# Optimization experiments

Hardware: AMD Instinct MI355X
Metric: run time of the kernel (lower is better)

## Reference

```python
import jax, jax.numpy as jnp
from jax import lax
import numpy as np

B, OBS, PRED, F, H = 2048, 20, 30, 16, 1024


def _lstm_layer(x, Wih, Whh, bih, bhh):
    # x: [T, B, in]; PyTorch gate order i, f, g, o; zero initial state
    Bb = x.shape[1]
    Hh = Whh.shape[1]
    def step(carry, xt):
        h, c = carry
        g = xt @ Wih.T + h @ Whh.T + bih + bhh
        i, f, gg, o = jnp.split(g, 4, axis=-1)
        c = jax.nn.sigmoid(f) * c + jax.nn.sigmoid(i) * jnp.tanh(gg)
        h = jax.nn.sigmoid(o) * jnp.tanh(c)
        return (h, c), h
    z = jnp.zeros((Bb, Hh), x.dtype)
    _, hs = lax.scan(step, (z, z), x)
    return hs  # [T, B, H]


def _lstm2(x, Wih0, Whh0, bih0, bhh0, Wih1, Whh1, bih1, bhh1):
    return _lstm_layer(_lstm_layer(x, Wih0, Whh0, bih0, bhh0), Wih1, Whh1, bih1, bhh1)


def setup_inputs() -> dict:
    key = jax.random.key(0)
    ks = jax.random.split(key, 32)
    s = 0.05
    def w(k, shape):
        return jax.random.normal(k, shape, dtype=jnp.float32) * s
    d = {
        'x_in': jax.random.normal(ks[0], (B, OBS, F), dtype=jnp.float32),
        'y': jax.random.normal(ks[1], (B, PRED, F), dtype=jnp.float32),
        'v_in': jax.random.normal(ks[2], (B, OBS, F), dtype=jnp.float32),
        'sx': jnp.ones((1,), jnp.float32),
        'sv': jnp.ones((1,), jnp.float32),
    }
    i = 3
    for p in ['v', 'a']:
        d[p + 'Wih0'] = w(ks[i], (4 * H, F)); i += 1
        d[p + 'Whh0'] = w(ks[i], (4 * H, H)); i += 1
        d[p + 'bih0'] = w(ks[i], (4 * H,)); i += 1
        d[p + 'bhh0'] = w(ks[i], (4 * H,)); i += 1
        d[p + 'Wih1'] = w(ks[i], (4 * H, H)); i += 1
        d[p + 'Whh1'] = w(ks[i], (4 * H, H)); i += 1
        d[p + 'bih1'] = w(ks[i], (4 * H,)); i += 1
        d[p + 'bhh1'] = w(ks[i], (4 * H,)); i += 1
        d[p + 'Wl'] = w(ks[i], (F, H)); i += 1
        d[p + 'bl'] = w(ks[i], (F,)); i += 1
    return d


def reference(x_in, y, v_in, sx, sv,
              vWih0, vWhh0, vbih0, vbhh0, vWih1, vWhh1, vbih1, vbhh1, vWl, vbl,
              aWih0, aWhh0, abih0, abhh0, aWih1, aWhh1, abih1, abhh1, aWl, abl):
    # last observed position, scaled: [1, B, F]
    x = jnp.transpose(x_in, (1, 0, 2))[-1:] * sx
    yT = sx * jnp.transpose(y, (1, 0, 2))  # [PRED, B, F]
    v_seq = jnp.transpose(v_in, (1, 0, 2))  # [OBS, B, F]
    a_seq = v_seq[1:] - v_seq[:-1]          # [OBS-1, B, F]

    vh = _lstm2(v_seq, vWih0, vWhh0, vbih0, vbhh0, vWih1, vWhh1, vbih1, vbhh1)
    v = sv * jnp.tanh(vh[-1:] @ vWl.T + vbl)  # [1, B, F]

    ah = _lstm2(a_seq, aWih0, aWhh0, abih0, abhh0, aWih1, aWhh1, abih1, abhh1)
    a = jnp.tanh(ah @ aWl.T + abl)[-1:]       # [1, B, F] (unscaled, fed back)

    v = v + sv * a
    x = x + v

    def body(carry, _):
        a, v, x = carry
        # NOTE: faithful to source -- LSTM state resets to zero each step
        ah = _lstm2(a, aWih0, aWhh0, abih0, abhh0, aWih1, aWhh1, abih1, abhh1)
        a = jnp.tanh(ah @ aWl.T + abl)
        v = v + sv * a
        x = x + v
        return (a, v, x), x[0]

    _, xs = lax.scan(body, (a, v, x), None, length=PRED - 1)  # xs: [PRED-1, B, F]
    out = jnp.concatenate([x, xs], axis=0)  # [PRED, B, F]
    return (out, yT)
```

## Files before the change

kernel.cpp:

```cpp
#include <hip/hip_runtime.h>


#define B_    2048
#define OBS_  20
#define PRED_ 30
#define F_    16
#define H_    1024
#define GN_   4096

typedef _Float16 f16;
typedef _Float16 f16x8 __attribute__((ext_vector_type(8)));
typedef _Float16 f16x4 __attribute__((ext_vector_type(4)));
typedef float    f32x4 __attribute__((ext_vector_type(4)));

__device__ __forceinline__ float fast_sigmoid(float x) {
  return 1.0f / (1.0f + __expf(-x));
}
__device__ __forceinline__ float fast_tanh(float x) {
  float ax = fabsf(x);
  float e  = __expf(-2.0f * ax);
  float r  = (1.0f - e) / (1.0f + e);
  return copysignf(r, x);
}

__device__ __forceinline__ void stageA512(f16* dst, const f16* Asrc, int b0, int k0, int tid) {
  int o  = tid * 16;
  int rr = o >> 6;
  int sp = (o >> 4) & 3;
  int sl = sp ^ ((rr >> 1) & 3);
  const f16* gp = Asrc + (size_t)(b0 + rr) * H_ + k0 + sl * 8;
  __builtin_amdgcn_global_load_lds(
      (const __attribute__((address_space(1))) void*)gp,
      (__attribute__((address_space(3))) void*)((char*)dst + o), 16, 0, 0);
}
__device__ __forceinline__ void stageB512(f16* dst, const f16* Wsrc, int j0, int k0, int tid) {
#pragma unroll
  for (int cc = 0; cc < 2; ++cc) {
    int o  = cc * 8192 + tid * 16;
    int rr = o >> 6;
    int sp = (o >> 4) & 3;
    int sl = sp ^ ((rr >> 1) & 3);
    int grow = (rr >> 6) * H_ + j0 + (rr & 63);
    const f16* gp = Wsrc + (size_t)grow * H_ + k0 + sl * 8;
    __builtin_amdgcn_global_load_lds(
        (const __attribute__((address_space(1))) void*)gp,
        (__attribute__((address_space(3))) void*)((char*)dst + o), 16, 0, 0);
  }
}

__device__ __forceinline__ void acc_init(f32x4 (&acc)[4][4], const float* bias, int jcol) {
#pragma unroll
  for (int g = 0; g < 4; ++g) {
    float bv = bias[g * H_ + jcol];
#pragma unroll
    for (int m = 0; m < 4; ++m) acc[m][g] = (f32x4){bv, bv, bv, bv};
  }
}

__device__ __forceinline__ void run_k16(f32x4 (&acc)[4][4], const f16* A16, const f16* W16,
    int b0, int j0, int wr, int wc, int lcol, int lkq)
{
  f16x8 za = {0, 0, 0, 0, 0, 0, 0, 0};
  f16x8 af[4], bf[4];
#pragma unroll
  for (int m = 0; m < 4; ++m) {
    if (lkq < 2) {
      int row = b0 + wr * 64 + m * 16 + lcol;
      af[m] = *(const f16x8*)(A16 + (size_t)row * 16 + lkq * 8);
    } else af[m] = za;
  }
#pragma unroll
  for (int g = 0; g < 4; ++g) {
    if (lkq < 2) {
      int row = g * H_ + j0 + wc * 16 + lcol;
      bf[g] = *(const f16x8*)(W16 + (size_t)row * 16 + lkq * 8);
    } else bf[g] = za;
  }
#pragma unroll
  for (int m = 0; m < 4; ++m)
#pragma unroll
    for (int g = 0; g < 4; ++g)
      acc[m][g] = __builtin_amdgcn_mfma_f32_16x16x32_f16(af[m], bf[g], acc[m][g], 0, 0, 0);
}

__device__ __forceinline__ void kstep_mfma(f32x4 (&acc)[4][4], const f16* lA, const f16* lB,
    int wr, int wc, int lcol, int lkq)
{
  f16x8 av[4], bw[4];
#pragma unroll
  for (int m = 0; m < 4; ++m) {
    int ar = wr * 64 + m * 16 + lcol;
    int sa = lkq ^ ((ar >> 1) & 3);
    av[m] = *(const f16x8*)&lA[ar * 32 + sa * 8];
  }
#pragma unroll
  for (int g = 0; g < 4; ++g) {
    int br = g * 64 + wc * 16 + lcol;
    int sb = lkq ^ ((br >> 1) & 3);
    bw[g] = *(const f16x8*)&lB[br * 32 + sb * 8];
  }
#pragma unroll
  for (int m = 0; m < 4; ++m)
#pragma unroll
    for (int g = 0; g < 4; ++g)
      acc[m][g] = __builtin_amdgcn_mfma_f32_16x16x32_f16(av[m], bw[g], acc[m][g], 0, 0, 0);
}

__device__ __forceinline__ void run_kloop(f32x4 (&acc)[4][4],
    f16 (*lA)[4096], f16 (*lB)[8192],
    const f16* A0, const f16* W0, const f16* A1, const f16* W1,
    int NT, int NTSW,
    int b0, int j0, int tid, int wr, int wc, int lcol, int lkq)
{
  int cur = 0;
  for (int t = 0; t < NT; ++t) {
    if (t + 1 < NT) {
      int tn = t + 1;
      const f16* As = (tn >= NTSW) ? A1 : A0;
      const f16* Ws = (tn >= NTSW) ? W1 : W0;
      int k0 = (tn & 31) * 32;
      stageA512(lA[cur ^ 1], As, b0, k0, tid);
      stageB512(lB[cur ^ 1], Ws, j0, k0, tid);
      asm volatile("s_waitcnt vmcnt(3)\n\ts_barrier" ::: "memory");
    } else {
      asm volatile("s_waitcnt vmcnt(0)\n\ts_barrier" ::: "memory");
    }
    kstep_mfma(acc, lA[cur], lB[cur], wr, wc, lcol, lkq);
    asm volatile("s_waitcnt lgkmcnt(0)\n\ts_barrier" ::: "memory");
    cur ^= 1;
  }
}

__device__ __forceinline__ void lstm_epi_g(f32x4 (&acc)[4][4], const float* cin, float* cout,
    f16* hout, int b0, int jcol, int wr, int lkq, int hasc, int writec)
{
#pragma unroll
  for (int m = 0; m < 4; ++m) {
    int brow0 = b0 + wr * 64 + m * 16 + lkq * 4;
#pragma unroll
    for (int r = 0; r < 4; ++r) {
      size_t bi = (size_t)(brow0 + r) * H_ + jcol;
      float gi = acc[m][0][r], gf = acc[m][1][r], gg = acc[m][2][r], go = acc[m][3][r];
      float cold = hasc ? cin[bi] : 0.0f;
      float cn = fast_sigmoid(gf) * cold + fast_sigmoid(gi) * fast_tanh(gg);
      float hv = fast_sigmoid(go) * fast_tanh(cn);
      if (writec) cout[bi] = cn;
      hout[bi] = (f16)hv;
    }
  }
}

struct StepArgs {
  const f16* A16; const f16* W16v; const f16* W16a;
  const f16* A0;  const f16* W0v;  const f16* W0a;
  const f16* A1;  const f16* W1v;  const f16* W1a;
  const float* bv; const float* ba;
  const float* cin; float* cout; f16* hout;
  int k16, nt, hasc, writec;
};

__device__ __forceinline__ void lstm_body(const StepArgs& p, f16 (*lA)[4096], f16 (*lB)[8192], int bi)
{
  const int tid = threadIdx.x, lane = tid & 63;
  const int wv = tid >> 6;
  const int wr = wv >> 2, wc = wv & 3;
  const int bm = bi >> 4, bn = bi & 15;
  const int b0 = bm * 128, j0 = bn * 64;
  const int ch = bm >> 4;
  const int lcol = lane & 15, lkq = lane >> 4;
  const int jcol = j0 + wc * 16 + lcol;

  const f16* W16 = ch ? p.W16a : p.W16v;
  const f16* W0  = ch ? p.W0a  : p.W0v;
  const f16* W1  = ch ? p.W1a  : p.W1v;
  const float* bias = ch ? p.ba : p.bv;

  if (p.nt) { stageA512(lA[0], p.A0, b0, 0, tid); stageB512(lB[0], W0, j0, 0, tid); }
  f32x4 acc[4][4];
  acc_init(acc, bias, jcol);
  if (p.k16) run_k16(acc, p.A16, W16, b0, j0, wr, wc, lcol, lkq);
  if (p.nt)
    run_kloop(acc, lA, lB, p.A0, W0, p.A1, W1, p.nt, 32, b0, j0, tid, wr, wc, lcol, lkq);
  lstm_epi_g(acc, p.cin, p.cout, p.hout, b0, jcol, wr, lkq, p.hasc, p.writec);
}

__global__ __launch_bounds__(512, 4)
void obs_pair(StepArgs rlong, StepArgs qshort, int split)
{
  __shared__ f16 lA[2][4096];
  __shared__ f16 lB[2][8192];
  int blk = blockIdx.x;
  if (blk < split) lstm_body(rlong, lA, lB, blk);
  else             lstm_body(qshort, lA, lB, blk - split);
}

__global__ __launch_bounds__(512, 2)
void scan_l1(const f16* __restrict__ h0, const f16* __restrict__ Wih1,
             const float* __restrict__ bias1, const float* __restrict__ Wl,
             float* __restrict__ ppart)
{
  __shared__ f16 lA[2][4096];
  __shared__ f16 lB[2][8192];
  __shared__ f16 hl[128 * 72];
  const int tid = threadIdx.x, lane = tid & 63;
  const int wv = tid >> 6;
  const int wr = wv >> 2, wc = wv & 3;
  const int bm = blockIdx.x >> 4, bn = blockIdx.x & 15;
  const int b0 = bm * 128, j0 = bn * 64;
  const int lcol = lane & 15, lkq = lane >> 4;
  const int jcol = j0 + wc * 16 + lcol;

  stageA512(lA[0], h0, b0, 0, tid);
  stageB512(lB[0], Wih1, j0, 0, tid);
  f32x4 acc[4][4];
  acc_init(acc, bias1, jcol);
  run_kloop(acc, lA, lB, h0, Wih1, nullptr, nullptr, 32, 32, b0, j0, tid, wr, wc, lcol, lkq);

  int jl = wc * 16 + lcol;
#pragma unroll
  for (int m = 0; m < 4; ++m) {
#pragma unroll
    for (int r = 0; r < 4; ++r) {
      int row = wr * 64 + m * 16 + lkq * 4 + r;
      float gi = acc[m][0][r], gg = acc[m][2][r], go = acc[m][3][r];
      float cn = fast_sigmoid(gi) * fast_tanh(gg);
      float hv = fast_sigmoid(go) * fast_tanh(cn);
      hl[row * 72 + jl] = (f16)hv;
    }
  }
  __syncthreads();

  const float* wp = Wl + (size_t)lcol * H_ + j0 + lkq * 8;
  f16x8 bf0, bf1;
#pragma unroll
  for (int e = 0; e < 8; ++e) { bf0[e] = (f16)wp[e]; bf1[e] = (f16)wp[32 + e]; }
  int arow = wv * 16 + lcol;
  f16x8 af0 = *(const f16x8*)&hl[arow * 72 + lkq * 8];
  f16x8 af1 = *(const f16x8*)&hl[arow * 72 + 32 + lkq * 8];
  f32x4 pc = {0, 0, 0, 0};
  pc = __builtin_amdgcn_mfma_f32_16x16x32_f16(af0, bf0, pc, 0, 0, 0);
  pc = __builtin_amdgcn_mfma_f32_16x16x32_f16(af1, bf1, pc, 0, 0, 0);
#pragma unroll
  for (int r = 0; r < 4; ++r) {
    int prow = b0 + wv * 16 + lkq * 4 + r;
    ppart[(size_t)prow * 256 + bn * 16 + lcol] = pc[r];
  }
}

template<int FIRST, int LAST>
__global__ __launch_bounds__(256, 4)
void scan_l0(const float* __restrict__ ppart, const f16* __restrict__ a16f,
             const float* __restrict__ bl, const float* __restrict__ sv,
             float* __restrict__ v_buf, float* __restrict__ x_buf,
             float* __restrict__ out_t,
             const float* __restrict__ bias0, const f16* __restrict__ Wih0,
             f16* __restrict__ h0out)
{
  __shared__ f16 a_lds[128 * 16];
  const int tid = threadIdx.x;
  const int bm = LAST ? (int)blockIdx.x : (int)(blockIdx.x >> 5);
  const int bn = LAST ? 0 : (int)(blockIdx.x & 31);
  const int b0 = bm * 128;

  const int ebase = tid * 8;
  const int erow  = ebase >> 4;
  const int ef0   = ebase & 15;
  float av[8];
  if (FIRST) {
    f16x8 a8 = *(const f16x8*)&a16f[(size_t)(b0 + erow) * 16 + ef0];
#pragma unroll
    for (int e = 0; e < 8; ++e) av[e] = (float)a8[e];
  } else {
    f32x4 s0 = {0, 0, 0, 0}, s1 = {0, 0, 0, 0};
    const float* pp = ppart + (size_t)(b0 + erow) * 256 + ef0;
#pragma unroll
    for (int sN = 0; sN < 16; ++sN) {
      s0 += *(const f32x4*)(pp + sN * 16);
      s1 += *(const f32x4*)(pp + sN * 16 + 4);
    }
#pragma unroll
    for (int e = 0; e < 4; ++e) av[e] = fast_tanh(s0[e] + bl[ef0 + e]);
#pragma unroll
    for (int e = 0; e < 4; ++e) av[4 + e] = fast_tanh(s1[e] + bl[ef0 + 4 + e]);
    if (bn == 0) {
      float svv = sv[0];
#pragma unroll
      for (int e = 0; e < 8; ++e) {
        int idx = (b0 + erow) * F_ + ef0 + e;
        float v = v_buf[idx] + svv * av[e];
        v_buf[idx] = v;
        float x = x_buf[idx] + v;
        x_buf[idx] = x;
        out_t[idx] = x;
      }
    }
  }

  if (!LAST) {
    f16x8 a8;
#pragma unroll
    for (int e = 0; e < 8; ++e) a8[e] = (f16)av[e];
    *(f16x8*)&a_lds[ebase] = a8;
    __syncthreads();

    const int lane = tid & 63;
    const int wv = tid >> 6, wr = wv >> 1, wc = wv & 1;
    const int lcol = lane & 15, lkq = lane >> 4;
    const int j0 = bn * 32, jcol = j0 + wc * 16 + lcol;
    f32x4 acc[4][4];
    acc_init(acc, bias0, jcol);
    f16x8 za = {0, 0, 0, 0, 0, 0, 0, 0};
    f16x8 af[4], bf[4];
#pragma unroll
    for (int m = 0; m < 4; ++m) {
      if (lkq < 2) {
        int arow = wr * 64 + m * 16 + lcol;
        af[m] = *(const f16x8*)&a_lds[arow * 16 + lkq * 8];
      } else af[m] = za;
    }
#pragma unroll
    for (int g = 0; g < 4; ++g) {
      if (lkq < 2) {
        int brow = g * H_ + j0 + wc * 16 + lcol;
        bf[g] = *(const f16x8*)(Wih0 + (size_t)brow * 16 + lkq * 8);
      } else bf[g] = za;
    }
#pragma unroll
    for (int m = 0; m < 4; ++m)
#pragma unroll
      for (int g = 0; g < 4; ++g)
        acc[m][g] = __builtin_amdgcn_mfma_f32_16x16x32_f16(af[m], bf[g], acc[m][g], 0, 0, 0);
    lstm_epi_g(acc, nullptr, nullptr, h0out, b0, jcol, wr, lkq, 0, 0);
  }
}

template<int MODE>
__global__ __launch_bounds__(256)
void proj_update(const f16* __restrict__ h1, const float* __restrict__ Wl,
                 const float* __restrict__ bl, const float* __restrict__ sv,
                 float* __restrict__ v_buf, float* __restrict__ x_buf,
                 float* __restrict__ out_t, f16* __restrict__ a16)
{
  __shared__ f16 lh[16 * 1024];
  const int b0r = blockIdx.x * 16;
  const int tid = threadIdx.x;
#pragma unroll
  for (int c = 0; c < 8; ++c) {
    int o = c * 256 + tid;
    *(f16x8*)&lh[o * 8] = *(const f16x8*)&h1[(size_t)b0r * 1024 + o * 8];
  }
  __syncthreads();
  const int br = tid >> 4;
  const int f  = tid & 15;
  float s0 = 0, s1 = 0, s2 = 0, s3 = 0;
  const float4* wp = (const float4*)(Wl + (size_t)f * 1024);
#pragma unroll 4
  for (int k8 = 0; k8 < 128; ++k8) {
    f16x8 hv = *(const f16x8*)&lh[br * 1024 + k8 * 8];
    float4 w0 = wp[k8 * 2], w1 = wp[k8 * 2 + 1];
    s0 += (float)hv[0] * w0.x + (float)hv[4] * w1.x;
    s1 += (float)hv[1] * w0.y + (float)hv[5] * w1.y;
    s2 += (float)hv[2] * w0.z + (float)hv[6] * w1.z;
    s3 += (float)hv[3] * w0.w + (float)hv[7] * w1.w;
  }
  float t = fast_tanh(bl[f] + ((s0 + s1) + (s2 + s3)));
  int idx = (b0r + br) * F_ + f;
  if (MODE == 0) {
    v_buf[idx] = sv[0] * t;
  } else {
    float v = v_buf[idx] + sv[0] * t;
    v_buf[idx] = v;
    float x = x_buf[idx] + v;
    x_buf[idx] = x;
    out_t[idx] = x;
    a16[idx] = (f16)t;
  }
}

__global__ void prep_kernel(const float* __restrict__ x_in, const float* __restrict__ y,
                            const float* __restrict__ v_in, const float* __restrict__ sx,
                            float* __restrict__ out, float* __restrict__ x_buf,
                            f16* __restrict__ m16)
{
  const float s = sx[0];
  int gid = blockIdx.x * blockDim.x + threadIdx.x;
  int gs  = gridDim.x * blockDim.x;
  for (int i = gid; i < B_ * OBS_ * F_; i += gs) {
    int b = i / (OBS_ * F_);
    int rem = i - b * (OBS_ * F_);
    int t = rem >> 4;
    int f = rem & 15;
    float v = v_in[i];
    m16[((size_t)t * 4096 + b) * F_ + f] = (f16)v;
    if (t < OBS_ - 1)
      m16[((size_t)t * 4096 + 2048 + b) * F_ + f] = (f16)(v_in[i + F_] - v);
  }
  for (int i = gid; i < PRED_ * B_ * F_; i += gs) {
    int t = i / (B_ * F_);
    int rem = i - t * (B_ * F_);
    int b = rem >> 4;
    int f = rem & 15;
    out[PRED_ * B_ * F_ + i] = s * y[(b * PRED_ + t) * F_ + f];
  }
  for (int i = gid; i < B_ * F_; i += gs) {
    int b = i >> 4;
    int f = i & 15;
    x_buf[i] = s * x_in[(b * OBS_ + (OBS_ - 1)) * F_ + f];
  }
}

struct ConvArgs {
  const float* src[8];
  f16*         dst[8];
  int          n[8];
  const float* b1[4];
  const float* b2[4];
  float*       bd[4];
};

__global__ void convw(ConvArgs a)
{
  int gid = blockIdx.x * blockDim.x + threadIdx.x;
  int gs  = gridDim.x * blockDim.x;
#pragma unroll
  for (int s = 0; s < 8; ++s) {
    int n4 = a.n[s] >> 2;
    for (int i = gid; i < n4; i += gs) {
      float4 v = ((const float4*)a.src[s])[i];
      f16x4 d = {(f16)v.x, (f16)v.y, (f16)v.z, (f16)v.w};
      ((f16x4*)a.dst[s])[i] = d;
    }
  }
#pragma unroll
  for (int s = 0; s < 4; ++s) {
    for (int i = gid; i < GN_; i += gs) a.bd[s][i] = a.b1[s][i] + a.b2[s][i];
  }
}

extern "C" void kernel_launch(void* const* d_in, const int* in_sizes, int n_in,
                              void* d_out, int out_size, void* d_ws, size_t ws_size,
                              hipStream_t stream)
{
  (void)in_sizes; (void)n_in; (void)out_size; (void)ws_size;

  const float* x_in  = (const float*)d_in[0];
  const float* y     = (const float*)d_in[1];
  const float* v_in  = (const float*)d_in[2];
  const float* sx    = (const float*)d_in[3];
  const float* sv    = (const float*)d_in[4];
  const float* vWih0 = (const float*)d_in[5];
  const float* vWhh0 = (const float*)d_in[6];
  const float* vbih0 = (const float*)d_in[7];
  const float* vbhh0 = (const float*)d_in[8];
  const float* vWih1 = (const float*)d_in[9];
  const float* vWhh1 = (const float*)d_in[10];
  const float* vbih1 = (const float*)d_in[11];
  const float* vbhh1 = (const float*)d_in[12];
  const float* vWl   = (const float*)d_in[13];
  const float* vbl   = (const float*)d_in[14];
  const float* aWih0 = (const float*)d_in[15];
  const float* aWhh0 = (const float*)d_in[16];
  const float* abih0 = (const float*)d_in[17];
  const float* abhh0 = (const float*)d_in[18];
  const float* aWih1 = (const float*)d_in[19];
  const float* aWhh1 = (const float*)d_in[20];
  const float* abih1 = (const float*)d_in[21];
  const float* abhh1 = (const float*)d_in[22];
  const float* aWl   = (const float*)d_in[23];
  const float* abl   = (const float*)d_in[24];
  float* out = (float*)d_out;

  char* ws = (char*)d_ws;
  size_t off = 0;
  auto alloc = [&](size_t bytes) {
    char* p = ws + off;
    off += (bytes + 255) & ~(size_t)255;
    return p;
  };
  f16* vWih0f = (f16*)alloc((size_t)GN_ * F_ * 2);
  f16* vWhh0f = (f16*)alloc((size_t)GN_ * H_ * 2);
  f16* vWih1f = (f16*)alloc((size_t)GN_ * H_ * 2);
  f16* vWhh1f = (f16*)alloc((size_t)GN_ * H_ * 2);
  f16* aWih0f = (f16*)alloc((size_t)GN_ * F_ * 2);
  f16* aWhh0f = (f16*)alloc((size_t)GN_ * H_ * 2);
  f16* aWih1f = (f16*)alloc((size_t)GN_ * H_ * 2);
  f16* aWhh1f = (f16*)alloc((size_t)GN_ * H_ * 2);
  float* vb0 = (float*)alloc(GN_ * 4);
  float* vb1 = (float*)alloc(GN_ * 4);
  float* ab0 = (float*)alloc(GN_ * 4);
  float* ab1 = (float*)alloc(GN_ * 4);
  f16* m16 = (f16*)alloc((size_t)OBS_ * 4096 * F_ * 2);
  f16* h0a = (f16*)alloc((size_t)4096 * H_ * 2);
  f16* h0b = (f16*)alloc((size_t)4096 * H_ * 2);
  f16* h1a = (f16*)alloc((size_t)4096 * H_ * 2);
  f16* h1b = (f16*)alloc((size_t)4096 * H_ * 2);
  float* c0 = (float*)alloc((size_t)4096 * H_ * 4);
  float* c1 = (float*)alloc((size_t)4096 * H_ * 4);
  f16* a16   = (f16*)alloc((size_t)B_ * F_ * 2);
  float* v_buf = (float*)alloc((size_t)B_ * F_ * 4);
  float* x_buf = (float*)alloc((size_t)B_ * F_ * 4);
  float* ppart = (float*)alloc((size_t)B_ * 16 * F_ * 4);

  ConvArgs ca;
  ca.src[0] = vWih0; ca.dst[0] = vWih0f; ca.n[0] = GN_ * F_;
  ca.src[1] = vWhh0; ca.dst[1] = vWhh0f; ca.n[1] = GN_ * H_;
  ca.src[2] = vWih1; ca.dst[2] = vWih1f; ca.n[2] = GN_ * H_;
  ca.src[3] = vWhh1; ca.dst[3] = vWhh1f; ca.n[3] = GN_ * H_;
  ca.src[4] = aWih0; ca.dst[4] = aWih0f; ca.n[4] = GN_ * F_;
  ca.src[5] = aWhh0; ca.dst[5] = aWhh0f; ca.n[5] = GN_ * H_;
  ca.src[6] = aWih1; ca.dst[6] = aWih1f; ca.n[6] = GN_ * H_;
  ca.src[7] = aWhh1; ca.dst[7] = aWhh1f; ca.n[7] = GN_ * H_;
  ca.b1[0] = vbih0; ca.b2[0] = vbhh0; ca.bd[0] = vb0;
  ca.b1[1] = vbih1; ca.b2[1] = vbhh1; ca.bd[1] = vb1;
  ca.b1[2] = abih0; ca.b2[2] = abhh0; ca.bd[2] = ab0;
  ca.b1[3] = abih1; ca.b2[3] = abhh1; ca.bd[3] = ab1;
  convw<<<1024, 256, 0, stream>>>(ca);
  prep_kernel<<<1024, 256, 0, stream>>>(x_in, y, v_in, sx, out, x_buf, m16);

  auto h0buf = [&](int t) { return (t & 1) ? h0b : h0a; };
  auto h1buf = [&](int t) { return (t & 1) ? h1b : h1a; };
  StepArgs dummy{};

  {
    StepArgs q{};
    q.A16 = m16; q.W16v = vWih0f; q.W16a = aWih0f;
    q.bv = vb0; q.ba = ab0;
    q.cout = c0; q.hout = h0buf(0);
    q.k16 = 1; q.nt = 0; q.hasc = 0; q.writec = 1;
    obs_pair<<<512, 512, 0, stream>>>(dummy, q, 0);
  }

  for (int t = 1; t < OBS_; ++t) {
    int u = t - 1;
    StepArgs q{};
    q.A16 = m16 + (size_t)t * 4096 * F_;
    q.W16v = vWih0f; q.W16a = aWih0f;
    q.A0 = h0buf(t - 1); q.W0v = vWhh0f; q.W0a = aWhh0f;
    q.bv = vb0; q.ba = ab0;
    q.cin = c0; q.cout = c0; q.hout = h0buf(t);
    q.k16 = 1; q.nt = 32; q.hasc = 1; q.writec = 1;

    StepArgs r{};
    r.A0 = h0buf(u); r.W0v = vWih1f; r.W0a = aWih1f;
    r.A1 = (u > 0) ? h1buf(u - 1) : nullptr;
    r.W1v = vWhh1f; r.W1a = aWhh1f;
    r.bv = vb1; r.ba = ab1;
    r.cin = c1; r.cout = c1; r.hout = h1buf(u);
    r.k16 = 0; r.nt = (u > 0) ? 64 : 32; r.hasc = (u > 0); r.writec = 1;

    int qblocks = (t == OBS_ - 1) ? 256 : 512;
    obs_pair<<<512 + qblocks, 512, 0, stream>>>(r, q, 512);
  }

  {
    StepArgs r{};
    r.A0 = h0buf(19); r.W0v = vWih1f; r.W0a = aWih1f;
    r.A1 = h1buf(18); r.W1v = vWhh1f; r.W1a = aWhh1f;
    r.bv = vb1; r.ba = ab1;
    r.cin = c1; r.cout = c1; r.hout = h1buf(19);
    r.k16 = 0; r.nt = 64; r.hasc = 1; r.writec = 1;
    obs_pair<<<256, 512, 0, stream>>>(r, dummy, 256);
  }

  proj_update<0><<<128, 256, 0, stream>>>(h1buf(19), vWl, vbl, sv,
                                          v_buf, nullptr, nullptr, nullptr);
  proj_update<1><<<128, 256, 0, stream>>>(h1buf(18) + (size_t)2048 * H_, aWl, abl, sv,
                                          v_buf, x_buf, out, a16);

  scan_l0<1, 0><<<512, 256, 0, stream>>>(ppart, a16, abl, sv, v_buf, x_buf, out,
                                         ab0, aWih0f, h0a);
  scan_l1<<<256, 512, 0, stream>>>(h0a, aWih1f, ab1, aWl, ppart);
  for (int t = 2; t < PRED_; ++t) {
    scan_l0<0, 0><<<512, 256, 0, stream>>>(ppart, nullptr, abl, sv, v_buf, x_buf,
                                           out + (size_t)(t - 1) * B_ * F_,
                                           ab0, aWih0f, h0a);
    scan_l1<<<256, 512, 0, stream>>>(h0a, aWih1f, ab1, aWl, ppart);
  }
  scan_l0<0, 1><<<16, 256, 0, stream>>>(ppart, nullptr, abl, sv, v_buf, x_buf,
                                        out + (size_t)(PRED_ - 1) * B_ * F_,
                                        ab0, aWih0f, h0a);
}
```

Baseline: 4.204 ms.

## Triple-buffer GEMM k-loop and interleave long/short LSTM blocks

The k-loop shared-memory pipeline goes from double to triple buffering, so loads are issued two k-steps ahead and the waitcnt thresholds change to match. This is meant to hide more global-load latency behind the MFMA work. The obs_pair kernel now interleaves layer-1 (long) and layer-0 (short) blocks in the launch order, which should balance work across CUs instead of putting all long blocks first. scan_l1 reuses the lA buffer for its h staging and raises its launch bound to 4, but the extra LDS per block (about 72KB) may reduce occupancy.

```diff
diff --git a/kernel.cpp b/kernel.cpp
--- a/kernel.cpp
+++ b/kernel.cpp
@@ -114,20 +114,23 @@
 {
   int cur = 0;
   for (int t = 0; t < NT; ++t) {
-    if (t + 1 < NT) {
-      int tn = t + 1;
+    if (t + 2 < NT) {
+      int tn = t + 2;
       const f16* As = (tn >= NTSW) ? A1 : A0;
       const f16* Ws = (tn >= NTSW) ? W1 : W0;
       int k0 = (tn & 31) * 32;
-      stageA512(lA[cur ^ 1], As, b0, k0, tid);
-      stageB512(lB[cur ^ 1], Ws, j0, k0, tid);
+      int wb = cur + 2; if (wb >= 3) wb -= 3;
+      stageA512(lA[wb], As, b0, k0, tid);
+      stageB512(lB[wb], Ws, j0, k0, tid);
+      asm volatile("s_waitcnt vmcnt(6)\n\ts_barrier" ::: "memory");
+    } else if (t + 1 < NT) {
       asm volatile("s_waitcnt vmcnt(3)\n\ts_barrier" ::: "memory");
     } else {
       asm volatile("s_waitcnt vmcnt(0)\n\ts_barrier" ::: "memory");
     }
     kstep_mfma(acc, lA[cur], lB[cur], wr, wc, lcol, lkq);
     asm volatile("s_waitcnt lgkmcnt(0)\n\ts_barrier" ::: "memory");
-    cur ^= 1;
+    if (++cur == 3) cur = 0;
   }
 }
 
@@ -175,7 +178,10 @@
   const f16* W1  = ch ? p.W1a  : p.W1v;
   const float* bias = ch ? p.ba : p.bv;
 
-  if (p.nt) { stageA512(lA[0], p.A0, b0, 0, tid); stageB512(lB[0], W0, j0, 0, tid); }
+  if (p.nt) {
+    stageA512(lA[0], p.A0, b0, 0, tid);  stageB512(lB[0], W0, j0, 0, tid);
+    stageA512(lA[1], p.A0, b0, 32, tid); stageB512(lB[1], W0, j0, 32, tid);
+  }
   f32x4 acc[4][4];
   acc_init(acc, bias, jcol);
   if (p.k16) run_k16(acc, p.A16, W16, b0, j0, wr, wc, lcol, lkq);
@@ -185,23 +191,27 @@
 }
 
 __global__ __launch_bounds__(512, 4)
-void obs_pair(StepArgs rlong, StepArgs qshort, int split)
-{
-  __shared__ f16 lA[2][4096];
-  __shared__ f16 lB[2][8192];
+void obs_pair(StepArgs rlong, StepArgs qshort, int nl, int ns)
+{
+  __shared__ f16 lA[3][4096];
+  __shared__ f16 lB[3][8192];
   int blk = blockIdx.x;
-  if (blk < split) lstm_body(rlong, lA, lB, blk);
-  else             lstm_body(qshort, lA, lB, blk - split);
-}
-
-__global__ __launch_bounds__(512, 2)
+  int li = -1, si = -1;
+  if (nl == 0)      si = blk;
+  else if (ns == 0) li = blk;
+  else if (blk < 2 * ns) { if (blk & 1) si = blk >> 1; else li = blk >> 1; }
+  else li = ns + (blk - 2 * ns);
+  if (li >= 0) lstm_body(rlong, lA, lB, li);
+  else         lstm_body(qshort, lA, lB, si);
+}
+
+__global__ __launch_bounds__(512, 4)
 void scan_l1(const f16* __restrict__ h0, const f16* __restrict__ Wih1,
              const float* __restrict__ bias1, const float* __restrict__ Wl,
              float* __restrict__ ppart)
 {
-  __shared__ f16 lA[2][4096];
-  __shared__ f16 lB[2][8192];
-  __shared__ f16 hl[128 * 72];
+  __shared__ f16 lA[3][4096];
+  __shared__ f16 lB[3][8192];
   const int tid = threadIdx.x, lane = tid & 63;
   const int wv = tid >> 6;
   const int wr = wv >> 2, wc = wv & 3;
@@ -210,12 +220,13 @@
   const int lcol = lane & 15, lkq = lane >> 4;
   const int jcol = j0 + wc * 16 + lcol;
 
-  stageA512(lA[0], h0, b0, 0, tid);
-  stageB512(lB[0], Wih1, j0, 0, tid);
+  stageA512(lA[0], h0, b0, 0, tid);  stageB512(lB[0], Wih1, j0, 0, tid);
+  stageA512(lA[1], h0, b0, 32, tid); stageB512(lB[1], Wih1, j0, 32, tid);
   f32x4 acc[4][4];
   acc_init(acc, bias1, jcol);
   run_kloop(acc, lA, lB, h0, Wih1, nullptr, nullptr, 32, 32, b0, j0, tid, wr, wc, lcol, lkq);
 
+  f16* hl = &lA[0][0];
   int jl = wc * 16 + lcol;
 #pragma unroll
   for (int m = 0; m < 4; ++m) {
@@ -527,7 +538,7 @@
     q.bv = vb0; q.ba = ab0;
     q.cout = c0; q.hout = h0buf(0);
     q.k16 = 1; q.nt = 0; q.hasc = 0; q.writec = 1;
-    obs_pair<<<512, 512, 0, stream>>>(dummy, q, 0);
+    obs_pair<<<512, 512, 0, stream>>>(dummy, q, 0, 512);
   }
 
   for (int t = 1; t < OBS_; ++t) {
@@ -548,8 +559,8 @@
     r.cin = c1; r.cout = c1; r.hout = h1buf(u);
     r.k16 = 0; r.nt = (u > 0) ? 64 : 32; r.hasc = (u > 0); r.writec = 1;
 
-    int qblocks = (t == OBS_ - 1) ? 256 : 512;
-    obs_pair<<<512 + qblocks, 512, 0, stream>>>(r, q, 512);
+    int ns = (t == OBS_ - 1) ? 256 : 512;
+    obs_pair<<<512 + ns, 512, 0, stream>>>(r, q, 512, ns);
   }
 
   {
@@ -559,7 +570,7 @@
     r.bv = vb1; r.ba = ab1;
     r.cin = c1; r.cout = c1; r.hout = h1buf(19);
     r.k16 = 0; r.nt = 64; r.hasc = 1; r.writec = 1;
-    obs_pair<<<256, 512, 0, stream>>>(r, dummy, 256);
+    obs_pair<<<256, 512, 0, stream>>>(r, dummy, 256, 0);
   }
 
   proj_update<0><<<128, 256, 0, stream>>>(h1buf(19), vWl, vbl, sv,
```

Result: no change. 4.264 ms (+1.4%).
